# Optimization experiments

Measured on AMD Instinct MI355X. Metric: run time of the kernel, lower is better.

## Reference

```python
import jax, jax.numpy as jnp
import numpy as np

INPUT_DIM = 1024
OUTPUT_DIM = 1000
DEPTH = 10
LAMBDA_REG = 1e-3
N_INTERNAL = 2 ** DEPTH - 1
N_LEAF = 2 ** DEPTH
BATCH = 16384


def setup_inputs() -> dict:
    key = jax.random.key(0)
    k1, k2, k3 = jax.random.split(key, 3)
    X = jax.random.normal(k1, (BATCH, INPUT_DIM), dtype=jnp.float32)
    # torch nn.Linear weight layout: [out_features, in_features]; scaled to keep
    # sigmoid routing probs away from 0/1 saturation (log-reg term).
    W_internal = jax.random.normal(k2, (N_INTERNAL, INPUT_DIM + 1), dtype=jnp.float32) * 0.02
    W_leaf = jax.random.normal(k3, (OUTPUT_DIM, N_LEAF), dtype=jnp.float32) * 0.02
    return {"X": X, "W_internal": W_internal, "W_leaf": W_leaf}


def _tree_paths(X, W_internal):
    B = X.shape[0]
    Xb = jnp.concatenate([jnp.ones((B, 1), X.dtype), X], axis=1)  # [B, D+1]
    logits = jax.nn.sigmoid(Xb @ W_internal.T)                    # [B, N_int]
    routing = jnp.stack([logits, 1.0 - logits], axis=2)           # [B, N_int, 2]
    path = jnp.ones((B, 1), X.dtype)
    reg = jnp.float32(0.0)
    start = 0
    for layer in range(DEPTH):
        n = 2 ** layer
        lp = routing[:, start:start + n, :].reshape(B, 2 * n)     # next_paths [B, 2n]
        path = jnp.repeat(path, 2, axis=1) * lp                   # new path probs [B, 2n]
        # Faithful to source: parent_idx = node_idx // 2 indexes the UPDATED path probs.
        parent = jnp.repeat(path[:, :n], 2, axis=1)               # [B, 2n]
        num = jnp.sum(lp * parent, axis=0)                        # [2n]
        den = jnp.sum(parent, axis=0) + 1e-8                      # [2n]
        alpha = num / den
        factor = LAMBDA_REG * 2.0 ** (-layer)
        reg = reg + factor * jnp.sum(-0.5 * (jnp.log(alpha) + jnp.log(1.0 - alpha)))
        start += n
    return path, reg  # path: [B, 2^DEPTH]


def reference(X, W_internal, W_leaf):
    path_probs, reg = _tree_paths(X, W_internal)
    predictions = path_probs @ W_leaf.T   # [B, output_dim]
    return predictions, reg
```

## Files before the change

### kernel.cpp

```cpp
#include <hip/hip_runtime.h>
#include <hip/hip_bf16.h>

#define B_ROWS 16384
#define K_DIM  1024
#define N_INT  1023
#define N_OUT  1000

using s8vec = __attribute__((ext_vector_type(8))) short;
using f32x4 = __attribute__((ext_vector_type(4))) float;

static const size_t OFF_XB   = 0;
static const size_t OFF_W1   = OFF_XB   + 33554432;
static const size_t OFF_BIAS = OFF_W1   + 2097152;
static const size_t OFF_PROB = OFF_BIAS + 4096;
static const size_t OFF_PATH = OFF_PROB + 33554432;
static const size_t OFF_W2   = OFF_PATH + 33554432;
static const size_t OFF_SG   = OFF_W2   + 2097152;

__device__ __forceinline__ float b2f(ushort u) {
  return __uint_as_float(((unsigned)u) << 16);
}
__device__ __forceinline__ float blo(unsigned u) { return __uint_as_float(u << 16); }
__device__ __forceinline__ float bhi(unsigned u) { return __uint_as_float(u & 0xffff0000u); }
__device__ __forceinline__ ushort f2b(float f) {
  unsigned u = __float_as_uint(f);
  u = u + 0x7FFFu + ((u >> 16) & 1u);
  return (ushort)(u >> 16);
}

__device__ __forceinline__ void load_lds16(const ushort* g, ushort* l) {
  __builtin_amdgcn_global_load_lds((const __attribute__((address_space(1))) void*)g,
                                   (__attribute__((address_space(3))) void*)l,
                                   16, 0, 0);
}

__global__ __launch_bounds__(256) void cvt_all(const float4* __restrict__ X,
                                               ushort4* __restrict__ O,
                                               const float* __restrict__ Wi,
                                               const float* __restrict__ Wl,
                                               ushort* __restrict__ W1,
                                               ushort* __restrict__ W2,
                                               float* __restrict__ bias) {
  const int b = blockIdx.x;
  if (b < 16384) {
    const int i = b * 256 + threadIdx.x;
    const float4 v = X[i];
    ushort4 o;
    o.x = f2b(v.x); o.y = f2b(v.y); o.z = f2b(v.z); o.w = f2b(v.w);
    O[i] = o;
  } else {
    const int idx = (b - 16384) * 256 + threadIdx.x;
    if (idx < (1 << 20)) {
      const int n = idx >> 10, k = idx & 1023;
      const float v = (n < N_INT) ? Wi[n * 1025 + 1 + k] : 0.f;
      W1[idx] = f2b(v);
      if (k == 0) bias[n] = (n < N_INT) ? Wi[n * 1025] : 0.f;
    } else {
      const int j = idx - (1 << 20);
      const int n = j >> 10, k = j & 1023;
      const float v = (n < N_OUT) ? Wl[n * 1024 + k] : 0.f;
      W2[j] = f2b(v);
    }
  }
}

template <int MODE>
__global__ __launch_bounds__(256, 4) void gemm_bt(const ushort* __restrict__ A,
                                                  const ushort* __restrict__ Bm,
                                                  const float* __restrict__ bias,
                                                  void* __restrict__ outp) {
  __shared__ ushort As[4096];
  __shared__ ushort Bs[4096];
  const int tid = threadIdx.x;
  const int bm = blockIdx.x, bn = blockIdx.y;
  const int lane = tid & 63, wv = tid >> 6;
  const int wm = wv >> 1, wn = wv & 1;
  const int m16 = lane & 15, q = lane >> 4;
  const int qs = q ^ ((m16 >> 1) & 3);

  const int r0 = tid >> 2;
  const int qsw = (tid & 3) ^ ((r0 >> 1) & 3);
  const ushort* aG = A  + (size_t)(bm * 128 + r0) * 1024 + qsw * 8;
  const ushort* bG = Bm + (size_t)(bn * 128 + r0) * 1024 + qsw * 8;
  ushort* AsW = As + wv * 512;
  ushort* BsW = Bs + wv * 512;

  f32x4 acc[4][4] = {};

  for (int k0 = 0; k0 < 1024; k0 += 32) {
    if (k0) __syncthreads();
    load_lds16(aG + k0, AsW);
    load_lds16(aG + 65536 + k0, AsW + 2048);
    load_lds16(bG + k0, BsW);
    load_lds16(bG + 65536 + k0, BsW + 2048);
    __syncthreads();

    s8vec af[4], bfv[4];
#pragma unroll
    for (int i = 0; i < 4; ++i)
      af[i] = *(const s8vec*)(As + (wm * 64 + i * 16 + m16) * 32 + qs * 8);
#pragma unroll
    for (int j = 0; j < 4; ++j)
      bfv[j] = *(const s8vec*)(Bs + (wn * 64 + j * 16 + m16) * 32 + qs * 8);
#pragma unroll
    for (int i = 0; i < 4; ++i)
#pragma unroll
      for (int j = 0; j < 4; ++j)
        acc[i][j] = __builtin_amdgcn_mfma_f32_16x16x32_bf16(af[i], bfv[j], acc[i][j], 0, 0, 0);
  }

  if (MODE == 0) {
    ushort* P = (ushort*)outp;
#pragma unroll
    for (int i = 0; i < 4; ++i)
#pragma unroll
      for (int r = 0; r < 4; ++r) {
        const int gr = bm * 128 + wm * 64 + i * 16 + q * 4 + r;
#pragma unroll
        for (int j = 0; j < 4; ++j) {
          const int gc = bn * 128 + wn * 64 + j * 16 + m16;
          const float z = acc[i][j][r] + bias[gc];
          const float p = 1.f / (1.f + expf(-z));
          if (gc < N_INT) P[(size_t)gr * 1024 + gc + 1] = f2b(p);
        }
      }
  } else {
    float* O = (float*)outp;
#pragma unroll
    for (int i = 0; i < 4; ++i)
#pragma unroll
      for (int r = 0; r < 4; ++r) {
        const int gr = bm * 128 + wm * 64 + i * 16 + q * 4 + r;
#pragma unroll
        for (int j = 0; j < 4; ++j) {
          const int gc = bn * 128 + wn * 64 + j * 16 + m16;
          if (gc < N_OUT) O[(size_t)gr * 1000 + gc] = acc[i][j][r];
        }
      }
  }
}

__global__ __launch_bounds__(256) void tree_kernel(const ushort* __restrict__ probs,
                                                   ushort* __restrict__ path) {
  const int lane = threadIdx.x & 63;
  const int r = blockIdx.x * 4 + (threadIdx.x >> 6);
  const ushort* prow = probs + (size_t)r * 1024;

  const int hh  = (int)prow[lane];
  const ushort p6 = prow[64 + lane];
  const uint   p7 = *(const uint*)(prow + 128 + 2 * lane);
  const uint2  p8 = *(const uint2*)(prow + 256 + 4 * lane);
  const uint4  p9 = *(const uint4*)(prow + 512 + 8 * lane);

  float v = 1.f;
#pragma unroll
  for (int t = 1; t <= 6; ++t) {
    const int ell = t - 1;
    const int e = lane >> (6 - t);
    const float p = b2f((ushort)__shfl(hh, (1 << ell) + (e >> 1)));
    v *= (e & 1) ? (1.f - p) : p;
  }

  float w[16];
  { const float p = b2f(p6); w[1] = v * (1.f - p); w[0] = v * p; }
  {
    const float pA = blo(p7), pB = bhi(p7);
    w[3] = w[1] * (1.f - pB); w[2] = w[1] * pB;
    w[1] = w[0] * (1.f - pA); w[0] = w[0] * pA;
  }
  {
    const float pv[4] = { blo(p8.x), bhi(p8.x), blo(p8.y), bhi(p8.y) };
#pragma unroll
    for (int i = 3; i >= 0; --i) {
      w[2 * i + 1] = w[i] * (1.f - pv[i]);
      w[2 * i]     = w[i] * pv[i];
    }
  }
  {
    const uint pv[4] = { p9.x, p9.y, p9.z, p9.w };
#pragma unroll
    for (int i = 7; i >= 0; --i) {
      const float p = (i & 1) ? bhi(pv[i >> 1]) : blo(pv[i >> 1]);
      w[2 * i + 1] = w[i] * (1.f - p);
      w[2 * i]     = w[i] * p;
    }
  }
  union { ushort u[16]; uint4 q4[2]; } pk;
#pragma unroll
  for (int i = 0; i < 16; ++i) pk.u[i] = f2b(w[i]);
  uint4* dst = (uint4*)(path + (size_t)r * 1024 + lane * 16);
  dst[0] = pk.q4[0];
  dst[1] = pk.q4[1];
}

__global__ __launch_bounds__(256) void accum_kernel(const ushort* __restrict__ probs,
                                                    const ushort* __restrict__ path,
                                                    float* __restrict__ Spart) {
  __shared__ float Ss[2048];
  for (int i = threadIdx.x; i < 2048; i += 256) Ss[i] = 0.f;
  __syncthreads();
  const int lane = threadIdx.x & 63;
  const int ll = lane & 31;
  const int half = lane >> 5;
  const int hb = half << 5;
  const int gw = blockIdx.x * 4 + (threadIdx.x >> 6);

  float a19[16] = {}, a29[16] = {};
  float a18[8]  = {}, a28[8]  = {};
  float a17[4]  = {}, a27[4]  = {};
  float a16[2]  = {}, a26[2]  = {};
  float t1[6] = {}, t2[6] = {};

#pragma unroll
  for (int it = 0; it < 2; ++it) {
    const int r = gw * 4 + it * 2 + half;
    const ushort* prow = probs + (size_t)r * 1024;
    const ushort* wrow = path  + (size_t)r * 1024;

    const int   hlo = (int)prow[ll];
    const float p5  = b2f(prow[32 + ll]);
    union { uint4 q[2]; ushort u[16]; } wl;
    wl.q[0] = *(const uint4*)(wrow + 16 * ll);
    wl.q[1] = *(const uint4*)(wrow + 16 * ll + 8);
    union { uint4 q[2]; ushort u[16]; } j9;
    j9.q[0] = *(const uint4*)(prow + 512 + 16 * ll);
    j9.q[1] = *(const uint4*)(prow + 512 + 16 * ll + 8);
    union { uint4 q; ushort u[8]; } j8;
    j8.q = *(const uint4*)(prow + 256 + 8 * ll);
    union { uint2 q; ushort u[4]; } j7;
    j7.q = *(const uint2*)(prow + 128 + 4 * ll);
    union { uint q; ushort u[2]; } j6;
    j6.q = *(const uint*)(prow + 64 + 2 * ll);

    float w[16];
#pragma unroll
    for (int i = 0; i < 16; ++i) w[i] = b2f(wl.u[i]);
    float L8[8], L7[4], L6[2];
#pragma unroll
    for (int i = 0; i < 8; ++i) L8[i] = w[2 * i] + w[2 * i + 1];
#pragma unroll
    for (int i = 0; i < 4; ++i) L7[i] = L8[2 * i] + L8[2 * i + 1];
    L6[0] = L7[0] + L7[1]; L6[1] = L7[2] + L7[3];
    const float T = L6[0] + L6[1];

#pragma unroll
    for (int i = 0; i < 16; ++i) { a19[i] += w[i];  a29[i] += b2f(j9.u[i]) * w[i]; }
#pragma unroll
    for (int i = 0; i < 8; ++i)  { a18[i] += L8[i]; a28[i] += b2f(j8.u[i]) * L8[i]; }
#pragma unroll
    for (int i = 0; i < 4; ++i)  { a17[i] += L7[i]; a27[i] += b2f(j7.u[i]) * L7[i]; }
#pragma unroll
    for (int i = 0; i < 2; ++i)  { a16[i] += L6[i]; a26[i] += b2f(j6.u[i]) * L6[i]; }

    t1[5] += T; t2[5] += p5 * T;
    const float T1 = T  + __shfl_xor(T, 1);
    const float T2 = T1 + __shfl_xor(T1, 2);
    const float T3 = T2 + __shfl_xor(T2, 4);
    const float T4 = T3 + __shfl_xor(T3, 8);
    const float T5 = T4 + __shfl_xor(T4, 16);
    const float v4 = __shfl(T1, hb | ((2 * ll) & 31));
    const float v3 = __shfl(T2, hb | ((4 * ll) & 31));
    const float v2 = __shfl(T3, hb | ((8 * ll) & 31));
    const float v1 = __shfl(T4, hb | ((16 * ll) & 31));
    const float q4 = b2f((ushort)__shfl(hlo, hb | ((16 + ll) & 31)));
    const float q3 = b2f((ushort)__shfl(hlo, hb | ((8 + ll) & 31)));
    const float q2 = b2f((ushort)__shfl(hlo, hb | ((4 + ll) & 31)));
    const float q1 = b2f((ushort)__shfl(hlo, hb | ((2 + ll) & 31)));
    const float q0 = b2f((ushort)__shfl(hlo, hb | 1));
    if (ll < 16) { t1[4] += v4; t2[4] += q4 * v4; }
    if (ll < 8)  { t1[3] += v3; t2[3] += q3 * v3; }
    if (ll < 4)  { t1[2] += v2; t2[2] += q2 * v2; }
    if (ll < 2)  { t1[1] += v1; t2[1] += q1 * v1; }
    if (ll < 1)  { t1[0] += T5; t2[0] += q0 * T5; }
  }

#pragma unroll
  for (int i = 0; i < 16; ++i) { a19[i] += __shfl_xor(a19[i], 32); a29[i] += __shfl_xor(a29[i], 32); }
#pragma unroll
  for (int i = 0; i < 8; ++i)  { a18[i] += __shfl_xor(a18[i], 32); a28[i] += __shfl_xor(a28[i], 32); }
#pragma unroll
  for (int i = 0; i < 4; ++i)  { a17[i] += __shfl_xor(a17[i], 32); a27[i] += __shfl_xor(a27[i], 32); }
#pragma unroll
  for (int i = 0; i < 2; ++i)  { a16[i] += __shfl_xor(a16[i], 32); a26[i] += __shfl_xor(a26[i], 32); }
#pragma unroll
  for (int i = 0; i < 6; ++i)  { t1[i] += __shfl_xor(t1[i], 32);   t2[i] += __shfl_xor(t2[i], 32); }

  if (lane < 32) {
#pragma unroll
    for (int i = 0; i < 16; ++i) { atomicAdd(&Ss[511 + 16 * ll + i], a19[i]); atomicAdd(&Ss[1535 + 16 * ll + i], a29[i]); }
#pragma unroll
    for (int i = 0; i < 8; ++i)  { atomicAdd(&Ss[255 + 8 * ll + i],  a18[i]); atomicAdd(&Ss[1279 + 8 * ll + i],  a28[i]); }
#pragma unroll
    for (int i = 0; i < 4; ++i)  { atomicAdd(&Ss[127 + 4 * ll + i],  a17[i]); atomicAdd(&Ss[1151 + 4 * ll + i],  a27[i]); }
#pragma unroll
    for (int i = 0; i < 2; ++i)  { atomicAdd(&Ss[63 + 2 * ll + i],   a16[i]); atomicAdd(&Ss[1087 + 2 * ll + i],  a26[i]); }
    atomicAdd(&Ss[31 + ll], t1[5]); atomicAdd(&Ss[1055 + ll], t2[5]);
    if (ll < 16) { atomicAdd(&Ss[15 + ll], t1[4]); atomicAdd(&Ss[1039 + ll], t2[4]); }
    if (ll < 8)  { atomicAdd(&Ss[7 + ll],  t1[3]); atomicAdd(&Ss[1031 + ll], t2[3]); }
    if (ll < 4)  { atomicAdd(&Ss[3 + ll],  t1[2]); atomicAdd(&Ss[1027 + ll], t2[2]); }
    if (ll < 2)  { atomicAdd(&Ss[1 + ll],  t1[1]); atomicAdd(&Ss[1025 + ll], t2[1]); }
    if (ll < 1)  { atomicAdd(&Ss[0],       t1[0]); atomicAdd(&Ss[1024],      t2[0]); }
  }
  __syncthreads();
  float* Sp = Spart + (size_t)blockIdx.x * 2048;
  for (int i = threadIdx.x; i < 2048; i += 256) Sp[i] = Ss[i];
}

__global__ __launch_bounds__(256) void reduce_kernel(const float* __restrict__ Spart,
                                                     float* __restrict__ Sg) {
  const int t = threadIdx.x;
  float acc[8] = {};
  const float* base = Spart + (size_t)blockIdx.x * 32 * 2048;
  for (int b = 0; b < 32; ++b) {
    const float* p = base + (size_t)b * 2048;
#pragma unroll
    for (int k = 0; k < 8; ++k) acc[k] += p[t + 256 * k];
  }
#pragma unroll
  for (int k = 0; k < 8; ++k) {
    const int i = t + 256 * k;
    const int node = i & 1023;
    if (node < 1023) atomicAdd(&Sg[(i < 1024 ? 0 : 2048) + node], acc[k]);
  }
}

__global__ __launch_bounds__(1024) void finalize_kernel(const float* __restrict__ Sg,
                                                        float* __restrict__ outreg) {
  const int tid = threadIdx.x;
  double val = 0.0;
  if (tid < 1023) {
    const int ell = 31 - __clz(tid + 1);
    const double s1 = (double)Sg[tid];
    const double s2 = (double)Sg[2048 + tid];
    const double den = s1 + 1e-8;
    const double a0 = s2 / den;
    const double a1 = (s1 - s2) / den;
    const double f = 1e-3 * (1.0 / (double)(1 << ell));
    val = -0.5 * f * (log(a0) + log(1.0 - a0) + log(a1) + log(1.0 - a1));
  }
#pragma unroll
  for (int o = 32; o > 0; o >>= 1) val += __shfl_down(val, o, 64);
  __shared__ double partd[16];
  if ((tid & 63) == 0) partd[tid >> 6] = val;
  __syncthreads();
  if (tid == 0) {
    double t = 0.0;
    for (int i = 0; i < 16; ++i) t += partd[i];
    outreg[0] = (float)t;
  }
}

extern "C" void kernel_launch(void* const* d_in, const int* in_sizes, int n_in,
                              void* d_out, int out_size, void* d_ws, size_t ws_size,
                              hipStream_t stream) {
  const float* X     = (const float*)d_in[0];
  const float* Wint  = (const float*)d_in[1];
  const float* Wleaf = (const float*)d_in[2];
  float* out = (float*)d_out;
  char* ws = (char*)d_ws;

  ushort* Xb   = (ushort*)(ws + OFF_XB);
  ushort* W1   = (ushort*)(ws + OFF_W1);
  float*  bias = (float*)(ws + OFF_BIAS);
  ushort* prob = (ushort*)(ws + OFF_PROB);
  ushort* path = (ushort*)(ws + OFF_PATH);
  ushort* W2   = (ushort*)(ws + OFF_W2);
  float*  Sg   = (float*)(ws + OFF_SG);
  float*  Spart = (float*)(ws + OFF_XB);

  (void)hipMemsetAsync(ws + OFF_SG, 0, 16384, stream);
  cvt_all<<<24576, 256, 0, stream>>>((const float4*)X, (ushort4*)Xb,
                                     Wint, Wleaf, W1, W2, bias);
  gemm_bt<0><<<dim3(128, 8), 256, 0, stream>>>(Xb, W1, bias, (void*)prob);
  tree_kernel<<<4096, 256, 0, stream>>>(prob, path);
  gemm_bt<1><<<dim3(128, 8), 256, 0, stream>>>(path, W2, nullptr, (void*)out);
  accum_kernel<<<1024, 256, 0, stream>>>(prob, path, Spart);
  reduce_kernel<<<32, 256, 0, stream>>>(Spart, Sg);
  finalize_kernel<<<1, 1024, 0, stream>>>(Sg, out + (size_t)B_ROWS * N_OUT);
}
```

Measured before the change: 307.2 us.

## Double-buffer LDS tiles in bf16 GEMM to overlap global loads with MFMA

Converts the GEMM main loop to a two-stage LDS ping-pong: the next K-slice is issued via direct-to-LDS loads while the current slice is consumed by MFMAs, with manual vmcnt waits and barriers replacing the two __syncthreads per iteration. This is meant to hide global memory latency behind compute. It doubles LDS usage per block to 32KB, which may cap occupancy at the requested 4 blocks per CU. It also relies on hand-written waitcnt/barrier asm whose correctness depends on the compiler's instruction ordering.

New measurement: 308.3 us. Within noise of the previous version (+0.3%).

```diff
diff --git a/kernel.cpp b/kernel.cpp
--- a/kernel.cpp
+++ b/kernel.cpp
@@ -69,8 +69,8 @@
                                                   const ushort* __restrict__ Bm,
                                                   const float* __restrict__ bias,
                                                   void* __restrict__ outp) {
-  __shared__ ushort As[4096];
-  __shared__ ushort Bs[4096];
+  __shared__ ushort As[2][4096];
+  __shared__ ushort Bs[2][4096];
   const int tid = threadIdx.x;
   const int bm = blockIdx.x, bn = blockIdx.y;
   const int lane = tid & 63, wv = tid >> 6;
@@ -82,32 +82,45 @@
   const int qsw = (tid & 3) ^ ((r0 >> 1) & 3);
   const ushort* aG = A  + (size_t)(bm * 128 + r0) * 1024 + qsw * 8;
   const ushort* bG = Bm + (size_t)(bn * 128 + r0) * 1024 + qsw * 8;
-  ushort* AsW = As + wv * 512;
-  ushort* BsW = Bs + wv * 512;
 
   f32x4 acc[4][4] = {};
 
-  for (int k0 = 0; k0 < 1024; k0 += 32) {
-    if (k0) __syncthreads();
-    load_lds16(aG + k0, AsW);
-    load_lds16(aG + 65536 + k0, AsW + 2048);
-    load_lds16(bG + k0, BsW);
-    load_lds16(bG + 65536 + k0, BsW + 2048);
-    __syncthreads();
-
-    s8vec af[4], bfv[4];
-#pragma unroll
-    for (int i = 0; i < 4; ++i)
-      af[i] = *(const s8vec*)(As + (wm * 64 + i * 16 + m16) * 32 + qs * 8);
-#pragma unroll
-    for (int j = 0; j < 4; ++j)
-      bfv[j] = *(const s8vec*)(Bs + (wn * 64 + j * 16 + m16) * 32 + qs * 8);
-#pragma unroll
-    for (int i = 0; i < 4; ++i)
-#pragma unroll
-      for (int j = 0; j < 4; ++j)
-        acc[i][j] = __builtin_amdgcn_mfma_f32_16x16x32_bf16(af[i], bfv[j], acc[i][j], 0, 0, 0);
-  }
+#define STAGE(buf, kk) do {                                   \
+    load_lds16(aG + (kk), As[buf] + wv * 512);                \
+    load_lds16(aG + 65536 + (kk), As[buf] + 2048 + wv * 512); \
+    load_lds16(bG + (kk), Bs[buf] + wv * 512);                \
+    load_lds16(bG + 65536 + (kk), Bs[buf] + 2048 + wv * 512); \
+  } while (0)
+
+#define COMPUTE(cur) do {                                                        \
+    s8vec af[4], bfv[4];                                                         \
+    _Pragma("unroll")                                                            \
+    for (int i = 0; i < 4; ++i)                                                  \
+      af[i] = *(const s8vec*)(As[cur] + (wm * 64 + i * 16 + m16) * 32 + qs * 8); \
+    _Pragma("unroll")                                                            \
+    for (int j = 0; j < 4; ++j)                                                  \
+      bfv[j] = *(const s8vec*)(Bs[cur] + (wn * 64 + j * 16 + m16) * 32 + qs * 8);\
+    _Pragma("unroll")                                                            \
+    for (int i = 0; i < 4; ++i)                                                  \
+      _Pragma("unroll")                                                          \
+      for (int j = 0; j < 4; ++j)                                                \
+        acc[i][j] = __builtin_amdgcn_mfma_f32_16x16x32_bf16(af[i], bfv[j],       \
+                                                            acc[i][j], 0, 0, 0);\
+  } while (0)
+
+  STAGE(0, 0);
+#pragma unroll 1
+  for (int k0 = 0; k0 < 992; k0 += 32) {
+    const int cur = (k0 >> 5) & 1;
+    STAGE(cur ^ 1, k0 + 32);
+    asm volatile("s_waitcnt vmcnt(4)\n\ts_barrier" ::: "memory");
+    COMPUTE(cur);
+    asm volatile("s_barrier" ::: "memory");
+  }
+  asm volatile("s_waitcnt vmcnt(0)\n\ts_barrier" ::: "memory");
+  COMPUTE(1);
+#undef STAGE
+#undef COMPUTE
 
   if (MODE == 0) {
     ushort* P = (ushort*)outp;
```

## Enlarge GEMM tiles to 256x256 with double-buffered LDS and priority-scheduled MFMA

Applied to the files above, without the earlier changes.

Both bf16 GEMMs move from 128x128 tiles with 4 waves to 256x256 tiles with 8 waves. The k-step grows to 64 and LDS is double-buffered, so global-to-LDS loads for the next stage overlap MFMA work on the current one, with manual waitcnt/barrier control and s_setprio around the MFMA bursts. The aim is higher arithmetic intensity and fewer per-k barriers, hiding load latency. The cost is 128KB of LDS and larger accumulator register pressure. Only 256 blocks are launched, which may underfill the 256 CUs and waste work on the padded edge tiles.

Result: faster. 298.7 us (-2.8%).

```diff
diff --git a/kernel.cpp b/kernel.cpp
--- a/kernel.cpp
+++ b/kernel.cpp
@@ -65,61 +65,103 @@
 }
 
 template <int MODE>
-__global__ __launch_bounds__(256, 4) void gemm_bt(const ushort* __restrict__ A,
+__global__ __launch_bounds__(512, 2) void gemm_bt(const ushort* __restrict__ A,
                                                   const ushort* __restrict__ Bm,
                                                   const float* __restrict__ bias,
                                                   void* __restrict__ outp) {
-  __shared__ ushort As[4096];
-  __shared__ ushort Bs[4096];
+  __shared__ ushort Al[2][16384];
+  __shared__ ushort Bl[2][16384];
   const int tid = threadIdx.x;
   const int bm = blockIdx.x, bn = blockIdx.y;
   const int lane = tid & 63, wv = tid >> 6;
-  const int wm = wv >> 1, wn = wv & 1;
+  const int wm = wv >> 2, wn = wv & 3;
   const int m16 = lane & 15, q = lane >> 4;
-  const int qs = q ^ ((m16 >> 1) & 3);
-
-  const int r0 = tid >> 2;
-  const int qsw = (tid & 3) ^ ((r0 >> 1) & 3);
-  const ushort* aG = A  + (size_t)(bm * 128 + r0) * 1024 + qsw * 8;
-  const ushort* bG = Bm + (size_t)(bn * 128 + r0) * 1024 + qsw * 8;
-  ushort* AsW = As + wv * 512;
-  ushort* BsW = Bs + wv * 512;
-
-  f32x4 acc[4][4] = {};
-
-  for (int k0 = 0; k0 < 1024; k0 += 32) {
-    if (k0) __syncthreads();
-    load_lds16(aG + k0, AsW);
-    load_lds16(aG + 65536 + k0, AsW + 2048);
-    load_lds16(bG + k0, BsW);
-    load_lds16(bG + 65536 + k0, BsW + 2048);
-    __syncthreads();
-
-    s8vec af[4], bfv[4];
-#pragma unroll
-    for (int i = 0; i < 4; ++i)
-      af[i] = *(const s8vec*)(As + (wm * 64 + i * 16 + m16) * 32 + qs * 8);
-#pragma unroll
-    for (int j = 0; j < 4; ++j)
-      bfv[j] = *(const s8vec*)(Bs + (wn * 64 + j * 16 + m16) * 32 + qs * 8);
-#pragma unroll
-    for (int i = 0; i < 4; ++i)
-#pragma unroll
-      for (int j = 0; j < 4; ++j)
-        acc[i][j] = __builtin_amdgcn_mfma_f32_16x16x32_bf16(af[i], bfv[j], acc[i][j], 0, 0, 0);
-  }
+  const int rs = m16 & 7;
+
+  const int qsw = (tid & 7) ^ ((tid >> 3) & 7);
+  const ushort* aGp = A  + (size_t)(bm * 256 + (tid >> 3)) * 1024 + qsw * 8;
+  const ushort* bGp = Bm + (size_t)(bn * 256 + (tid >> 3)) * 1024 + qsw * 8;
+
+  f32x4 acc[8][4] = {};
+  s8vec af[8], bf[4];
+
+#define STAGE_KT(b, kc) do {                                      \
+    load_lds16(aGp + (kc),          &Al[b][wv * 512]);            \
+    load_lds16(aGp + 65536 + (kc),  &Al[b][4096  + wv * 512]);    \
+    load_lds16(aGp + 131072 + (kc), &Al[b][8192  + wv * 512]);    \
+    load_lds16(aGp + 196608 + (kc), &Al[b][12288 + wv * 512]);    \
+    load_lds16(bGp + (kc),          &Bl[b][wv * 512]);            \
+    load_lds16(bGp + 65536 + (kc),  &Bl[b][4096  + wv * 512]);    \
+    load_lds16(bGp + 131072 + (kc), &Bl[b][8192  + wv * 512]);    \
+    load_lds16(bGp + 196608 + (kc), &Bl[b][12288 + wv * 512]);    \
+  } while (0)
+
+#define READF(b, c) do {                                                              \
+    _Pragma("unroll")                                                                 \
+    for (int mi = 0; mi < 8; ++mi)                                                    \
+      af[mi] = *(const s8vec*)(&Al[b][(wm * 128 + mi * 16 + m16) * 64 +               \
+                                      (((c) + q) ^ rs) * 8]);                         \
+    _Pragma("unroll")                                                                 \
+    for (int ni = 0; ni < 4; ++ni)                                                    \
+      bf[ni] = *(const s8vec*)(&Bl[b][(wn * 64 + ni * 16 + m16) * 64 +                \
+                                      (((c) + q) ^ rs) * 8]);                         \
+  } while (0)
+
+#define MF() do {                                                                     \
+    __builtin_amdgcn_s_setprio(1);                                                    \
+    _Pragma("unroll")                                                                 \
+    for (int mi = 0; mi < 8; ++mi)                                                    \
+      _Pragma("unroll")                                                               \
+      for (int ni = 0; ni < 4; ++ni)                                                  \
+        acc[mi][ni] = __builtin_amdgcn_mfma_f32_16x16x32_bf16(af[mi], bf[ni],         \
+                                                              acc[mi][ni], 0, 0, 0);  \
+    __builtin_amdgcn_s_setprio(0);                                                    \
+  } while (0)
+
+  STAGE_KT(0, 0);
+  STAGE_KT(1, 64);
+
+#pragma unroll 1
+  for (int it = 0; it < 7; ++it) {
+    const int kc0 = it * 128;
+    asm volatile("s_waitcnt vmcnt(8)\n\ts_barrier" ::: "memory");
+    READF(0, 0); MF();
+    READF(0, 4);
+    __builtin_amdgcn_sched_barrier(0);
+    asm volatile("s_waitcnt lgkmcnt(0)" ::: "memory");
+    asm volatile("s_barrier" ::: "memory");
+    STAGE_KT(0, kc0 + 128);
+    MF();
+    asm volatile("s_waitcnt vmcnt(8)\n\ts_barrier" ::: "memory");
+    READF(1, 0); MF();
+    READF(1, 4);
+    __builtin_amdgcn_sched_barrier(0);
+    asm volatile("s_waitcnt lgkmcnt(0)" ::: "memory");
+    asm volatile("s_barrier" ::: "memory");
+    STAGE_KT(1, kc0 + 192);
+    MF();
+  }
+  asm volatile("s_waitcnt vmcnt(8)\n\ts_barrier" ::: "memory");
+  READF(0, 0); MF();
+  READF(0, 4); MF();
+  asm volatile("s_waitcnt vmcnt(0)\n\ts_barrier" ::: "memory");
+  READF(1, 0); MF();
+  READF(1, 4); MF();
+#undef STAGE_KT
+#undef READF
+#undef MF
 
   if (MODE == 0) {
     ushort* P = (ushort*)outp;
 #pragma unroll
-    for (int i = 0; i < 4; ++i)
+    for (int mi = 0; mi < 8; ++mi)
 #pragma unroll
       for (int r = 0; r < 4; ++r) {
-        const int gr = bm * 128 + wm * 64 + i * 16 + q * 4 + r;
-#pragma unroll
-        for (int j = 0; j < 4; ++j) {
-          const int gc = bn * 128 + wn * 64 + j * 16 + m16;
-          const float z = acc[i][j][r] + bias[gc];
+        const int gr = bm * 256 + wm * 128 + mi * 16 + q * 4 + r;
+#pragma unroll
+        for (int ni = 0; ni < 4; ++ni) {
+          const int gc = bn * 256 + wn * 64 + ni * 16 + m16;
+          const float z = acc[mi][ni][r] + bias[gc];
           const float p = 1.f / (1.f + expf(-z));
           if (gc < N_INT) P[(size_t)gr * 1024 + gc + 1] = f2b(p);
         }
@@ -127,14 +169,14 @@
   } else {
     float* O = (float*)outp;
 #pragma unroll
-    for (int i = 0; i < 4; ++i)
+    for (int mi = 0; mi < 8; ++mi)
 #pragma unroll
       for (int r = 0; r < 4; ++r) {
-        const int gr = bm * 128 + wm * 64 + i * 16 + q * 4 + r;
-#pragma unroll
-        for (int j = 0; j < 4; ++j) {
-          const int gc = bn * 128 + wn * 64 + j * 16 + m16;
-          if (gc < N_OUT) O[(size_t)gr * 1000 + gc] = acc[i][j][r];
+        const int gr = bm * 256 + wm * 128 + mi * 16 + q * 4 + r;
+#pragma unroll
+        for (int ni = 0; ni < 4; ++ni) {
+          const int gc = bn * 256 + wn * 64 + ni * 16 + m16;
+          if (gc < N_OUT) O[(size_t)gr * 1000 + gc] = acc[mi][ni][r];
         }
       }
   }
@@ -371,9 +413,9 @@
   (void)hipMemsetAsync(ws + OFF_SG, 0, 16384, stream);
   cvt_all<<<24576, 256, 0, stream>>>((const float4*)X, (ushort4*)Xb,
                                      Wint, Wleaf, W1, W2, bias);
-  gemm_bt<0><<<dim3(128, 8), 256, 0, stream>>>(Xb, W1, bias, (void*)prob);
+  gemm_bt<0><<<dim3(64, 4), 512, 0, stream>>>(Xb, W1, bias, (void*)prob);
   tree_kernel<<<4096, 256, 0, stream>>>(prob, path);
-  gemm_bt<1><<<dim3(128, 8), 256, 0, stream>>>(path, W2, nullptr, (void*)out);
+  gemm_bt<1><<<dim3(64, 4), 512, 0, stream>>>(path, W2, nullptr, (void*)out);
   accum_kernel<<<1024, 256, 0, stream>>>(prob, path, Spart);
   reduce_kernel<<<32, 256, 0, stream>>>(Spart, Sg);
   finalize_kernel<<<1, 1024, 0, stream>>>(Sg, out + (size_t)B_ROWS * N_OUT);
```
